# Kernel optimization log

Measured on AMD Instinct MI355X. Metric: run time of the kernel, lower is better.

## Reference

```python
import jax, jax.numpy as jnp
import numpy as np

B, S, IN_DIM, D, H, L, C = 8, 1024, 256, 1024, 16, 6, 10
DK = D // H
EPS = 1e-5


def setup_inputs() -> dict:
    key = jax.random.key(0)
    ks = iter(jax.random.split(key, 64))
    n = lambda shape, s=0.02: jax.random.normal(next(ks), shape, dtype=jnp.float32) * s
    inp = {
        'x': jax.random.normal(next(ks), (B, S, IN_DIM), dtype=jnp.float32),
        'emb_w': n((IN_DIM, D)), 'emb_b': jnp.zeros((D,), jnp.float32),
        'Wq': n((L, D, D)), 'bq': jnp.zeros((L, D), jnp.float32),
        'Wk': n((L, D, D)), 'bk': jnp.zeros((L, D), jnp.float32),
        'Wv': n((L, D, D)), 'bv': jnp.zeros((L, D), jnp.float32),
        'Wo': n((L, D, D)), 'bo': jnp.zeros((L, D), jnp.float32),
        'W1': n((L, D, 4 * D)), 'b1': jnp.zeros((L, 4 * D), jnp.float32),
        'W2': n((L, 4 * D, D)), 'b2': jnp.zeros((L, D), jnp.float32),
        'ln1_s': jnp.ones((L, D), jnp.float32), 'ln1_b': jnp.zeros((L, D), jnp.float32),
        'ln2_s': jnp.ones((L, D), jnp.float32), 'ln2_b': jnp.zeros((L, D), jnp.float32),
        'fc_w': n((D, C)), 'fc_b': jnp.zeros((C,), jnp.float32),
    }
    return inp


def _pos_encoding_rows(n_rows):
    # Faithful to the torch module: pe is [max_len,1,D]; pe[:x.size(0)] picks the
    # first `batch` positions and broadcasts over the sequence dim.
    pos = jnp.arange(n_rows, dtype=jnp.float32)[:, None]
    div = jnp.exp(jnp.arange(0, D, 2, dtype=jnp.float32) * (-np.log(10000.0) / D))
    pe = jnp.zeros((n_rows, D), jnp.float32)
    pe = pe.at[:, 0::2].set(jnp.sin(pos * div)).at[:, 1::2].set(jnp.cos(pos * div))
    return pe


def _layer_norm(x, scale, bias):
    mu = jnp.mean(x, axis=-1, keepdims=True)
    var = jnp.mean(jnp.square(x - mu), axis=-1, keepdims=True)
    return (x - mu) * jax.lax.rsqrt(var + EPS) * scale + bias


def reference(x, emb_w, emb_b, Wq, bq, Wk, bk, Wv, bv, Wo, bo,
              W1, b1, W2, b2, ln1_s, ln1_b, ln2_s, ln2_b, fc_w, fc_b):
    h = x @ emb_w + emb_b                              # [B,S,D]
    h = h + _pos_encoding_rows(B)[:, None, :]          # broadcast pe[:B] over seq
    scale = 1.0 / np.sqrt(DK)
    for i in range(L):
        def heads(y, W, b):
            return (y @ W + b).reshape(B, S, H, DK).transpose(0, 2, 1, 3)  # bhsd
        q = heads(h, Wq[i], bq[i])
        k = heads(h, Wk[i], bk[i])
        v = heads(h, Wv[i], bv[i])
        scores = jnp.einsum('bhqd,bhkd->bhqk', q, k) * scale
        p = jax.nn.softmax(scores, axis=-1)
        o = jnp.einsum('bhqk,bhkd->bhqd', p, v)
        o = o.transpose(0, 2, 1, 3).reshape(B, S, D)
        attn_out = o @ Wo[i] + bo[i]
        h = _layer_norm(h + attn_out, ln1_s[i], ln1_b[i])
        ff = jax.nn.relu(h @ W1[i] + b1[i]) @ W2[i] + b2[i]
        h = _layer_norm(h + ff, ln2_s[i], ln2_b[i])
    pooled = jnp.mean(h, axis=1)                       # [B,D]
    return pooled @ fc_w + fc_b                        # [B,C]
```

## Files before the change

kernel.cpp:

```cpp
#include <hip/hip_runtime.h>
#include <stdint.h>

#define B_   8
#define S_   1024
#define IND  256
#define D_   1024
#define H_   16
#define DKH  64
#define L_   6
#define FF   4096
#define NTOK (B_*S_)

typedef __bf16 bf16;
typedef __attribute__((ext_vector_type(4))) float  f32x4;
typedef __attribute__((ext_vector_type(8))) __bf16 bf16x8;
typedef __attribute__((ext_vector_type(4))) __bf16 bf16x4;
typedef __attribute__((ext_vector_type(2))) __bf16 bf16x2;

#define AS1 __attribute__((address_space(1)))
#define AS3 __attribute__((address_space(3)))

__device__ __forceinline__ void gload16(const void* g, void* l) {
  __builtin_amdgcn_global_load_lds((AS1 void*)(const_cast<void*>(g)), (AS3 void*)l, 16, 0, 0);
}

__global__ __launch_bounds__(256)
void k_trans(const float* __restrict__ in, bf16* __restrict__ out,
             int K, int N, long inStride, long outStride) {
  __shared__ float t[32][33];
  const float* inp = in + (long)blockIdx.z * inStride;
  bf16* outp = out + (long)blockIdx.z * outStride;
  const int n0 = blockIdx.x * 32, k0 = blockIdx.y * 32;
  const int tx = threadIdx.x & 31, ty = threadIdx.x >> 5;
  #pragma unroll
  for (int j = 0; j < 32; j += 8)
    t[ty + j][tx] = inp[(long)(k0 + ty + j) * N + n0 + tx];
  __syncthreads();
  #pragma unroll
  for (int j = 0; j < 32; j += 8)
    outp[(long)(n0 + ty + j) * K + k0 + tx] = (bf16)t[tx][ty + j];
}

__global__ __launch_bounds__(256)
void k_f2b(const float* __restrict__ in, bf16* __restrict__ out) {
  const long i = ((long)blockIdx.x * 256 + threadIdx.x) * 4;
  f32x4 v = *(const f32x4*)(in + i);
  bf16x4 o;
  #pragma unroll
  for (int j = 0; j < 4; ++j) o[j] = (bf16)v[j];
  *(bf16x4*)(out + i) = o;
}

__global__ __launch_bounds__(256)
void k_pe(float* __restrict__ pe) {
  const int i = blockIdx.x * 256 + threadIdx.x;
  const int b = i >> 10, d = i & 1023;
  const float k2 = (float)(d & ~1);
  const float dv = __expf(k2 * (-9.210340371976184f / (float)D_));
  const float a = (float)b * dv;
  pe[i] = (d & 1) ? cosf(a) : sinf(a);
}

__global__ __launch_bounds__(256)
void k_packb(const float* __restrict__ bq, const float* __restrict__ bk,
             const float* __restrict__ bv, float* __restrict__ out) {
  const int i = blockIdx.x * 256 + threadIdx.x;
  const int l = i / 3072, j = i % 3072;
  const float* src = (j < 1024) ? bq : ((j < 2048) ? bk : bv);
  out[i] = src[l * 1024 + (j & 1023)];
}

template<int EPI>
__global__ __launch_bounds__(256)
void k_gemm(const bf16* __restrict__ A, const bf16* __restrict__ Bt,
            const float* __restrict__ bias,
            void* __restrict__ out0, void* __restrict__ out1,
            const float* __restrict__ pe,
            int M, int N, int K) {
  __shared__ __align__(16) bf16 sA[128 * 32];
  __shared__ __align__(16) bf16 sB[128 * 32];
  const int tid = threadIdx.x;
  const int lane = tid & 63, wv = tid >> 6;
  const int bx = blockIdx.x, by = blockIdx.y;
  const int wm = wv >> 1, wn = wv & 1;
  const int lg = lane >> 4, lc = lane & 15;
  const long arow0 = (long)by * 128;
  const long brow0 = (long)bx * 128;
  const int c0 = (wv * 2 + 0) * 64 + lane;
  const int c1 = (wv * 2 + 1) * 64 + lane;
  const int r0 = c0 >> 2, s0 = c0 & 3;
  const int r1 = c1 >> 2, s1 = c1 & 3;
  bf16* ldsA0 = sA + (wv * 2 + 0) * 512;
  bf16* ldsA1 = sA + (wv * 2 + 1) * 512;
  bf16* ldsB0 = sB + (wv * 2 + 0) * 512;
  bf16* ldsB1 = sB + (wv * 2 + 1) * 512;
  const bf16* Ab = A + arow0 * K;
  const bf16* Bb = Bt + brow0 * K;
  f32x4 acc[4][4] = {};
  const int kT = K >> 5;
  for (int kt = 0; kt < kT; ++kt) {
    const int k0 = kt << 5;
    gload16(Ab + (long)r0 * K + k0 + s0 * 8, ldsA0);
    gload16(Ab + (long)r1 * K + k0 + s1 * 8, ldsA1);
    gload16(Bb + (long)r0 * K + k0 + s0 * 8, ldsB0);
    gload16(Bb + (long)r1 * K + k0 + s1 * 8, ldsB1);
    __syncthreads();
    bf16x8 af[4], bfr[4];
    #pragma unroll
    for (int mr = 0; mr < 4; ++mr)
      af[mr] = *(const bf16x8*)(sA + (wm * 64 + mr * 16 + lc) * 32 + lg * 8);
    #pragma unroll
    for (int nc = 0; nc < 4; ++nc)
      bfr[nc] = *(const bf16x8*)(sB + (wn * 64 + nc * 16 + lc) * 32 + lg * 8);
    #pragma unroll
    for (int mr = 0; mr < 4; ++mr)
      #pragma unroll
      for (int nc = 0; nc < 4; ++nc)
        acc[mr][nc] = __builtin_amdgcn_mfma_f32_16x16x32_bf16(af[mr], bfr[nc], acc[mr][nc], 0, 0, 0);
    __syncthreads();
  }
  #pragma unroll
  for (int mr = 0; mr < 4; ++mr) {
    const int row0 = by * 128 + wm * 64 + mr * 16 + lg * 4;
    #pragma unroll
    for (int nc = 0; nc < 4; ++nc) {
      const int col = bx * 128 + wn * 64 + nc * 16 + lc;
      const float bvv = bias[col];
      #pragma unroll
      for (int r = 0; r < 4; ++r) {
        float v = acc[mr][nc][r] + bvv;
        const long rr = row0 + r;
        if constexpr (EPI == 0) {
          ((bf16*)out0)[rr * N + col] = (bf16)v;
        } else {
          const long bb = rr >> 10;
          v += pe[bb * D_ + col];
          ((float*)out0)[rr * N + col] = v;
          ((bf16*)out1)[rr * N + col] = (bf16)v;
        }
      }
    }
  }
}

template<int EPI>
__global__ __launch_bounds__(512, 2)
void k_gemm256(const bf16* __restrict__ A, const bf16* __restrict__ Bt,
               const float* __restrict__ bias,
               void* __restrict__ out0, void* __restrict__ out1,
               int M, int N, int K) {
  __shared__ __align__(16) bf16 lds[65536];
  const int tid = threadIdx.x;
  const int lane = tid & 63, wv = tid >> 6;
  const int wm = wv >> 2, wn = wv & 3;
  const int lg = lane >> 4, lc = lane & 15;
  const int tileRow = blockIdx.y * 256, tileCol = blockIdx.x * 256;
  const bf16* Abase = A + (long)tileRow * K;
  const bf16* Bbase = Bt + (long)tileCol * K;
  const long laneOff = (long)lc * K + lg * 8;
  f32x4 acc[8][4] = {};
  const int NT = K >> 6;
  const int NI = NT >> 1;

  auto stA = [&](int t, int h, int bb) {
    const int rg = h * 16 + wv * 2;
    const int mb = rg >> 1;
    const bf16* s = Abase + (long)(mb * 16) * K + t * 64 + laneOff;
    bf16* d = lds + bb * 32768 + rg * 512;
    gload16(s, d);
    gload16(s + 32, d + 512);
  };
  auto stB = [&](int t, int h, int bb) {
    const int rg = h * 16 + wv * 2;
    const int mb = rg >> 1;
    const bf16* s = Bbase + (long)(mb * 16) * K + t * 64 + laneOff;
    bf16* d = lds + bb * 32768 + 16384 + rg * 512;
    gload16(s, d);
    gload16(s + 32, d + 512);
  };

  bf16x8 aF[8];
  bf16x8 bF0[4], bF1[4];

#define LDA(BB, MH) do { _Pragma("unroll") for (int m = 0; m < 4; ++m) \
    _Pragma("unroll") for (int kk = 0; kk < 2; ++kk) \
      aF[m*2+kk] = *(const bf16x8*)(lds + (BB)*32768 + ((wm*8 + (MH)*4 + m)*2 + kk)*512 + lane*8); \
  } while(0)
#define LDB(BB, NH, DST) do { _Pragma("unroll") for (int n = 0; n < 2; ++n) \
    _Pragma("unroll") for (int kk = 0; kk < 2; ++kk) \
      DST[n*2+kk] = *(const bf16x8*)(lds + (BB)*32768 + 16384 + ((wn*4 + (NH)*2 + n)*2 + kk)*512 + lane*8); \
  } while(0)
#define MM(MH, NH, BSRC, VM) do { \
    if ((VM) == 1) asm volatile("s_waitcnt vmcnt(4)" ::: "memory"); \
    if ((VM) == 2) asm volatile("s_waitcnt vmcnt(0)" ::: "memory"); \
    __builtin_amdgcn_s_barrier(); \
    __builtin_amdgcn_s_setprio(1); \
    _Pragma("unroll") for (int m = 0; m < 4; ++m) \
      _Pragma("unroll") for (int n = 0; n < 2; ++n) { \
        acc[(MH)*4+m][(NH)*2+n] = __builtin_amdgcn_mfma_f32_16x16x32_bf16(aF[m*2+0], BSRC[n*2+0], acc[(MH)*4+m][(NH)*2+n], 0, 0, 0); \
        acc[(MH)*4+m][(NH)*2+n] = __builtin_amdgcn_mfma_f32_16x16x32_bf16(aF[m*2+1], BSRC[n*2+1], acc[(MH)*4+m][(NH)*2+n], 0, 0, 0); \
      } \
    __builtin_amdgcn_s_setprio(0); \
    __builtin_amdgcn_s_barrier(); \
  } while(0)

  stA(0, 0, 0); stB(0, 0, 0); stA(0, 1, 0); stB(0, 1, 0);
  if (NT > 1) { stA(1, 0, 1); stB(1, 0, 1); }
  asm volatile("s_waitcnt vmcnt(4)" ::: "memory");
  __builtin_amdgcn_s_barrier();

  for (int i = 0; i < NI - 1; ++i) {
    const int t1 = 2 * i + 1, t2 = 2 * i + 2, t3 = 2 * i + 3;
    LDA(0, 0); LDB(0, 0, bF0); stA(t1, 1, 1); MM(0, 0, bF0, 0);
    LDB(0, 1, bF1);            stB(t1, 1, 1); MM(0, 1, bF1, 0);
    LDA(0, 1);                 stA(t2, 0, 0); MM(1, 0, bF0, 0);
                               stB(t2, 0, 0); MM(1, 1, bF1, 1);
    LDA(1, 0); LDB(1, 0, bF0); stA(t2, 1, 0); MM(0, 0, bF0, 0);
    LDB(1, 1, bF1);            stB(t2, 1, 0); MM(0, 1, bF1, 0);
    LDA(1, 1);                 stA(t3, 0, 1); MM(1, 0, bF0, 0);
                               stB(t3, 0, 1); MM(1, 1, bF1, 1);
  }
  {
    const int t1 = NT - 1;
    LDA(0, 0); LDB(0, 0, bF0); stA(t1, 1, 1); MM(0, 0, bF0, 0);
    LDB(0, 1, bF1);            stB(t1, 1, 1); MM(0, 1, bF1, 0);
    LDA(0, 1);                                MM(1, 0, bF0, 0);
                                              MM(1, 1, bF1, 2);
    LDA(1, 0); LDB(1, 0, bF0);                MM(0, 0, bF0, 0);
    LDB(1, 1, bF1);                           MM(0, 1, bF1, 0);
    LDA(1, 1);                                MM(1, 0, bF0, 0);
                                              MM(1, 1, bF1, 0);
  }
#undef LDA
#undef LDB
#undef MM

  #pragma unroll
  for (int mr = 0; mr < 8; ++mr) {
    const int row0 = tileRow + wm * 128 + mr * 16 + lg * 4;
    #pragma unroll
    for (int nr = 0; nr < 4; ++nr) {
      const int col = tileCol + wn * 64 + nr * 16 + lc;
      const float bvv = bias[col];
      if constexpr (EPI == 2) {
        const int which = col >> 10;
        const int hh = (col & 1023) >> 6;
        const int dk = col & 63;
        const long bb = row0 >> 10;
        const int sr = row0 & 1023;
        if (which == 2) {
          bf16x4 pk;
          #pragma unroll
          for (int r = 0; r < 4; ++r) pk[r] = (bf16)(acc[mr][nr][r] + bvv);
          *(bf16x4*)((bf16*)out1 + ((bb * H_ + hh) * (long)DKH + dk) * S_ + sr) = pk;
        } else {
          #pragma unroll
          for (int r = 0; r < 4; ++r) {
            float v = acc[mr][nr][r] + bvv;
            if (which == 0) v *= 0.125f;
            ((bf16*)out0)[(long)which * NTOK * D_ + ((bb * H_ + hh) * (long)S_ + sr + r) * DKH + dk] = (bf16)v;
          }
        }
      } else {
        #pragma unroll
        for (int r = 0; r < 4; ++r) {
          float v = acc[mr][nr][r] + bvv;
          const long rr = row0 + r;
          if constexpr (EPI == 1) v = fmaxf(v, 0.f);
          ((bf16*)out0)[rr * N + col] = (bf16)v;
        }
      }
    }
  }
}

__global__ __launch_bounds__(256)
void k_flash(const bf16* __restrict__ qg, const bf16* __restrict__ kgl,
             const bf16* __restrict__ vtg, bf16* __restrict__ og) {
  __shared__ __align__(16) bf16 sK[64 * 64];
  __shared__ __align__(16) bf16 sV[64 * 64];
  __shared__ __align__(16) bf16 sP[4 * 16 * 64];
  const int tid = threadIdx.x, lane = tid & 63, wv = tid >> 6;
  const int lg = lane >> 4, lc = lane & 15;
  const int bh = blockIdx.y, qt = blockIdx.x;
  const long base = (long)bh * S_ * DKH;
  const bf16* qb = qg + base;
  const bf16* kb = kgl + base;
  const bf16* vb = vtg + base;
  const int qrow = qt * 64 + wv * 16 + lc;
  const bf16x8 qf0 = *(const bf16x8*)(qb + (long)qrow * DKH + lg * 8);
  const bf16x8 qf1 = *(const bf16x8*)(qb + (long)qrow * DKH + 32 + lg * 8);
  float mrun = -3e38f, lrun = 0.f;
  f32x4 oacc[4] = {};
  bf16* sPw = sP + wv * (16 * 64);
  const int swzP = (lc & 7) << 4;
  const int c0 = wv * 128 + lane, c1 = c0 + 64;
  const int r0 = c0 >> 3, sl0 = (c0 & 7) ^ (r0 & 7);
  const int r1 = c1 >> 3, sl1 = (c1 & 7) ^ (r1 & 7);
  bf16* dst0 = sK + c0 * 8 - lane * 8;
  bf16* dst1 = sK + c1 * 8 - lane * 8;
  bf16* dstV0 = sV + c0 * 8 - lane * 8;
  bf16* dstV1 = sV + c1 * 8 - lane * 8;
  for (int kt = 0; kt < S_ / 64; ++kt) {
    const int gk = kt * 64;
    gload16(kb + (long)(gk + r0) * DKH + sl0 * 8, dst0);
    gload16(kb + (long)(gk + r1) * DKH + sl1 * 8, dst1);
    gload16(vb + (long)r0 * S_ + gk + sl0 * 8, dstV0);
    gload16(vb + (long)r1 * S_ + gk + sl1 * 8, dstV1);
    __syncthreads();
    f32x4 sacc[4] = {};
    #pragma unroll
    for (int nc = 0; nc < 4; ++nc) {
      const int kr = nc * 16 + lc;
      bf16x8 k0 = *(const bf16x8*)((char*)sK + kr * 128 + (((0 + lg) ^ (kr & 7)) << 4));
      bf16x8 k1 = *(const bf16x8*)((char*)sK + kr * 128 + (((4 + lg) ^ (kr & 7)) << 4));
      sacc[nc] = __builtin_amdgcn_mfma_f32_16x16x32_bf16(k0, qf0, sacc[nc], 0, 0, 0);
      sacc[nc] = __builtin_amdgcn_mfma_f32_16x16x32_bf16(k1, qf1, sacc[nc], 0, 0, 0);
    }
    float pm = sacc[0][0];
    #pragma unroll
    for (int nc = 0; nc < 4; ++nc)
      #pragma unroll
      for (int r = 0; r < 4; ++r) pm = fmaxf(pm, sacc[nc][r]);
    pm = fmaxf(pm, __shfl_xor(pm, 16));
    pm = fmaxf(pm, __shfl_xor(pm, 32));
    const float mnew = fmaxf(mrun, pm);
    const float fac = __expf(mrun - mnew);
    float ps = 0.f;
    #pragma unroll
    for (int nc = 0; nc < 4; ++nc)
      #pragma unroll
      for (int r = 0; r < 4; ++r) {
        const float p = __expf(sacc[nc][r] - mnew);
        sacc[nc][r] = p;
        ps += p;
      }
    ps += __shfl_xor(ps, 16);
    ps += __shfl_xor(ps, 32);
    lrun = lrun * fac + ps;
    mrun = mnew;
    #pragma unroll
    for (int nc = 0; nc < 4; ++nc)
      #pragma unroll
      for (int rp = 0; rp < 2; ++rp) {
        bf16x2 t;
        t[0] = (bf16)sacc[nc][rp * 2 + 0];
        t[1] = (bf16)sacc[nc][rp * 2 + 1];
        *(bf16x2*)((char*)sPw + lc * 128 + ((nc * 32 + lg * 8 + rp * 4) ^ swzP)) = t;
      }
    asm volatile("s_waitcnt lgkmcnt(0)" ::: "memory");
    __builtin_amdgcn_sched_barrier(0);
    float fr[4];
    #pragma unroll
    for (int r = 0; r < 4; ++r) fr[r] = __shfl(fac, lg * 4 + r);
    #pragma unroll
    for (int nc = 0; nc < 4; ++nc)
      #pragma unroll
      for (int r = 0; r < 4; ++r) oacc[nc][r] *= fr[r];
    #pragma unroll
    for (int m = 0; m < 2; ++m) {
      const bf16x8 pf = *(const bf16x8*)((char*)sPw + lc * 128 + ((m * 64 + lg * 16) ^ swzP));
      #pragma unroll
      for (int nc = 0; nc < 4; ++nc) {
        const int vr = nc * 16 + lc;
        bf16x8 vf = *(const bf16x8*)((char*)sV + vr * 128 + (((m * 4 + lg) ^ (vr & 7)) << 4));
        oacc[nc] = __builtin_amdgcn_mfma_f32_16x16x32_bf16(pf, vf, oacc[nc], 0, 0, 0);
      }
    }
    __syncthreads();
  }
  const int b = bh >> 4, h = bh & 15;
  const float linv = 1.f / lrun;
  #pragma unroll
  for (int r = 0; r < 4; ++r) {
    const float inv = __shfl(linv, lg * 4 + r);
    const int s = qt * 64 + wv * 16 + lg * 4 + r;
    const long obase = (((long)b * S_ + s) * H_ + h) * DKH;
    #pragma unroll
    for (int nc = 0; nc < 4; ++nc)
      og[obase + nc * 16 + lc] = (bf16)(oacc[nc][r] * inv);
  }
}

__global__ __launch_bounds__(256)
void k_addln(const float* __restrict__ hin, const bf16* __restrict__ dlt,
             const float* __restrict__ sc, const float* __restrict__ bi,
             float* __restrict__ hout, bf16* __restrict__ hbout) {
  const int row = blockIdx.x, t = threadIdx.x;
  const long off = (long)row * D_ + t * 4;
  f32x4 hv = *(const f32x4*)(hin + off);
  bf16x4 dv = *(const bf16x4*)(dlt + off);
  f32x4 x;
  float s = 0.f, ss = 0.f;
  #pragma unroll
  for (int j = 0; j < 4; ++j) { x[j] = hv[j] + (float)dv[j]; s += x[j]; ss += x[j] * x[j]; }
  #pragma unroll
  for (int m = 1; m < 64; m <<= 1) { s += __shfl_xor(s, m); ss += __shfl_xor(ss, m); }
  __shared__ float red[8];
  const int w = t >> 6, ln = t & 63;
  if (ln == 0) { red[w] = s; red[4 + w] = ss; }
  __syncthreads();
  s = red[0] + red[1] + red[2] + red[3];
  ss = red[4] + red[5] + red[6] + red[7];
  const float mu = s * (1.f / D_);
  const float rstd = rsqrtf(ss * (1.f / D_) - mu * mu + 1e-5f);
  f32x4 scv = *(const f32x4*)(sc + t * 4);
  f32x4 biv = *(const f32x4*)(bi + t * 4);
  f32x4 y; bf16x4 yb;
  #pragma unroll
  for (int j = 0; j < 4; ++j) { y[j] = (x[j] - mu) * rstd * scv[j] + biv[j]; yb[j] = (bf16)y[j]; }
  *(f32x4*)(hout + off) = y;
  *(bf16x4*)(hbout + off) = yb;
}

__global__ __launch_bounds__(256)
void k_pool1(const float* __restrict__ h, float* __restrict__ part) {
  const int i = blockIdx.x * 256 + threadIdx.x;
  const int b = i >> 10, d = i & 1023;
  const int s0 = blockIdx.y * 128;
  float s = 0.f;
  for (int t = 0; t < 128; ++t) s += h[((long)b * S_ + s0 + t) * D_ + d];
  part[(long)blockIdx.y * NTOK + i] = s;
}

__global__ __launch_bounds__(256)
void k_pool2(const float* __restrict__ part, float* __restrict__ pooled) {
  const int i = blockIdx.x * 256 + threadIdx.x;
  float s = 0.f;
  #pragma unroll
  for (int j = 0; j < 8; ++j) s += part[(long)j * NTOK + i];
  pooled[i] = s * (1.f / S_);
}

__global__ __launch_bounds__(64)
void k_fc(const float* __restrict__ pooled, const float* __restrict__ fw,
          const float* __restrict__ fb, float* __restrict__ out) {
  const int b = blockIdx.x / 10, c = blockIdx.x % 10;
  const int lane = threadIdx.x;
  float s = 0.f;
  for (int d = lane; d < D_; d += 64) s += pooled[b * D_ + d] * fw[d * 10 + c];
  #pragma unroll
  for (int m = 1; m < 64; m <<= 1) s += __shfl_xor(s, m);
  if (lane == 0) out[b * 10 + c] = s + fb[c];
}

extern "C" void kernel_launch(void* const* d_in, const int* in_sizes, int n_in,
                              void* d_out, int out_size, void* d_ws, size_t ws_size,
                              hipStream_t stream) {
  const float* x     = (const float*)d_in[0];
  const float* emb_w = (const float*)d_in[1];
  const float* emb_b = (const float*)d_in[2];
  const float* Wq    = (const float*)d_in[3];
  const float* bq    = (const float*)d_in[4];
  const float* Wk    = (const float*)d_in[5];
  const float* bk    = (const float*)d_in[6];
  const float* Wv    = (const float*)d_in[7];
  const float* bv    = (const float*)d_in[8];
  const float* Wo    = (const float*)d_in[9];
  const float* bo    = (const float*)d_in[10];
  const float* W1    = (const float*)d_in[11];
  const float* b1    = (const float*)d_in[12];
  const float* W2    = (const float*)d_in[13];
  const float* b2    = (const float*)d_in[14];
  const float* ln1s  = (const float*)d_in[15];
  const float* ln1b  = (const float*)d_in[16];
  const float* ln2s  = (const float*)d_in[17];
  const float* ln2b  = (const float*)d_in[18];
  const float* fcw   = (const float*)d_in[19];
  const float* fcb   = (const float*)d_in[20];

  char* w = (char*)d_ws;
  size_t off = 0;
  auto alloc = [&](size_t bytes) -> char* {
    char* p = w + off;
    off += (bytes + 255) & ~(size_t)255;
    return p;
  };
  bf16*  x_bf  = (bf16*) alloc((size_t)NTOK * IND * 2);
  bf16*  embT  = (bf16*) alloc((size_t)D_ * IND * 2);
  bf16*  qkvT  = (bf16*) alloc((size_t)L_ * 3 * D_ * D_ * 2);
  bf16*  woT   = (bf16*) alloc((size_t)L_ * D_ * D_ * 2);
  bf16*  w1T   = (bf16*) alloc((size_t)L_ * FF * D_ * 2);
  bf16*  w2T   = (bf16*) alloc((size_t)L_ * D_ * FF * 2);
  float* qkvB  = (float*)alloc((size_t)L_ * 3 * D_ * 4);
  float* pe    = (float*)alloc((size_t)B_ * D_ * 4);
  float* h_f   = (float*)alloc((size_t)NTOK * D_ * 4);
  bf16*  h_b   = (bf16*) alloc((size_t)NTOK * D_ * 2);
  bf16*  delta = (bf16*) alloc((size_t)NTOK * D_ * 2);
  float* pooled= (float*)alloc((size_t)B_ * D_ * 4);
  float* part  = (float*)alloc((size_t)8 * NTOK * 4);
  bf16*  scratch = (bf16*)alloc((size_t)NTOK * FF * 2);
  bf16* qb  = scratch;
  bf16* kb  = scratch + (size_t)NTOK * D_;
  bf16* vTb = scratch + (size_t)2 * NTOK * D_;
  bf16* ob  = scratch + (size_t)3 * NTOK * D_;
  bf16* ffn1 = scratch;
  (void)ws_size; (void)in_sizes; (void)n_in; (void)out_size;

  k_f2b<<<dim3(NTOK * IND / 1024), dim3(256), 0, stream>>>(x, x_bf);
  k_trans<<<dim3(D_ / 32, IND / 32, 1), dim3(256), 0, stream>>>(emb_w, embT, IND, D_, 0, 0);
  k_trans<<<dim3(32, 32, L_), dim3(256), 0, stream>>>(Wq, qkvT,               D_, D_, (long)D_ * D_, (long)3 * D_ * D_);
  k_trans<<<dim3(32, 32, L_), dim3(256), 0, stream>>>(Wk, qkvT + D_ * D_,     D_, D_, (long)D_ * D_, (long)3 * D_ * D_);
  k_trans<<<dim3(32, 32, L_), dim3(256), 0, stream>>>(Wv, qkvT + 2 * D_ * D_, D_, D_, (long)D_ * D_, (long)3 * D_ * D_);
  k_trans<<<dim3(32, 32, L_), dim3(256), 0, stream>>>(Wo, woT, D_, D_, (long)D_ * D_, (long)D_ * D_);
  k_trans<<<dim3(FF / 32, 32, L_), dim3(256), 0, stream>>>(W1, w1T, D_, FF, (long)D_ * FF, (long)FF * D_);
  k_trans<<<dim3(32, FF / 32, L_), dim3(256), 0, stream>>>(W2, w2T, FF, D_, (long)FF * D_, (long)D_ * FF);
  k_pe<<<dim3(B_ * D_ / 256), dim3(256), 0, stream>>>(pe);
  k_packb<<<dim3(L_ * 3 * D_ / 256), dim3(256), 0, stream>>>(bq, bk, bv, qkvB);

  k_gemm<3><<<dim3(D_ / 128, NTOK / 128), dim3(256), 0, stream>>>(
      x_bf, embT, emb_b, h_f, h_b, pe, NTOK, D_, IND);

  for (int l = 0; l < L_; ++l) {
    k_gemm256<2><<<dim3(3 * D_ / 256, NTOK / 256), dim3(512), 0, stream>>>(
        h_b, qkvT + (size_t)l * 3 * D_ * D_, qkvB + l * 3 * D_,
        qb, vTb, NTOK, 3 * D_, D_);
    k_flash<<<dim3(S_ / 64, B_ * H_), dim3(256), 0, stream>>>(qb, kb, vTb, ob);
    k_gemm256<0><<<dim3(D_ / 256, NTOK / 256), dim3(512), 0, stream>>>(
        ob, woT + (size_t)l * D_ * D_, bo + l * D_,
        delta, nullptr, NTOK, D_, D_);
    k_addln<<<dim3(NTOK), dim3(256), 0, stream>>>(h_f, delta, ln1s + l * D_, ln1b + l * D_, h_f, h_b);
    k_gemm256<1><<<dim3(FF / 256, NTOK / 256), dim3(512), 0, stream>>>(
        h_b, w1T + (size_t)l * FF * D_, b1 + l * FF,
        ffn1, nullptr, NTOK, FF, D_);
    k_gemm256<0><<<dim3(D_ / 256, NTOK / 256), dim3(512), 0, stream>>>(
        ffn1, w2T + (size_t)l * D_ * FF, b2 + l * D_,
        delta, nullptr, NTOK, D_, FF);
    k_addln<<<dim3(NTOK), dim3(256), 0, stream>>>(h_f, delta, ln2s + l * D_, ln2b + l * D_, h_f, h_b);
  }

  k_pool1<<<dim3(NTOK / 256, 8), dim3(256), 0, stream>>>(h_f, part);
  k_pool2<<<dim3(NTOK / 256), dim3(256), 0, stream>>>(part, pooled);
  k_fc<<<dim3(B_ * 10), dim3(64), 0, stream>>>(pooled, fcw, fcb, (float*)d_out);
}
```

Baseline: 2.656 ms.

## Remap workgroups for XCD locality, retile N=1024 GEMMs, deepen 256-tile prefetch

Adds an XCD-aware block-index remap to both GEMM kernels and the flash-attention kernel, so consecutive tiles land on the same chiplet and share L2. The N=1024 GEMMs (Wo and W2) move from 256x256 tiles (128 blocks) to 128x128 tiles (512 blocks) to fill more CUs. The 256-tile GEMM pipeline is reordered to prefetch a full K-tile ahead, using vmcnt(8) waits and fewer barriers. The 128-tile GEMM also gets a new LDS layout matching the 256 kernel's fragment layout. The trade-offs are that smaller tiles lower data reuse per block, and the W2 GEMM with K=4096 runs on a simple kernel with no double buffering.

```diff
diff --git a/kernel.cpp b/kernel.cpp
--- a/kernel.cpp
+++ b/kernel.cpp
@@ -72,59 +72,57 @@
 
 template<int EPI>
 __global__ __launch_bounds__(256)
-void k_gemm(const bf16* __restrict__ A, const bf16* __restrict__ Bt,
-            const float* __restrict__ bias,
-            void* __restrict__ out0, void* __restrict__ out1,
-            const float* __restrict__ pe,
-            int M, int N, int K) {
+void k_gemm128(const bf16* __restrict__ A, const bf16* __restrict__ Bt,
+               const float* __restrict__ bias,
+               void* __restrict__ out0, void* __restrict__ out1,
+               const float* __restrict__ pe,
+               int M, int N, int K) {
   __shared__ __align__(16) bf16 sA[128 * 32];
   __shared__ __align__(16) bf16 sB[128 * 32];
-  const int tid = threadIdx.x;
-  const int lane = tid & 63, wv = tid >> 6;
-  const int bx = blockIdx.x, by = blockIdx.y;
+  const int tid = threadIdx.x, lane = tid & 63, wv = tid >> 6;
   const int wm = wv >> 1, wn = wv & 1;
   const int lg = lane >> 4, lc = lane & 15;
-  const long arow0 = (long)by * 128;
-  const long brow0 = (long)bx * 128;
-  const int c0 = (wv * 2 + 0) * 64 + lane;
-  const int c1 = (wv * 2 + 1) * 64 + lane;
-  const int r0 = c0 >> 2, s0 = c0 & 3;
-  const int r1 = c1 >> 2, s1 = c1 & 3;
-  bf16* ldsA0 = sA + (wv * 2 + 0) * 512;
-  bf16* ldsA1 = sA + (wv * 2 + 1) * 512;
-  bf16* ldsB0 = sB + (wv * 2 + 0) * 512;
-  bf16* ldsB1 = sB + (wv * 2 + 1) * 512;
-  const bf16* Ab = A + arow0 * K;
-  const bf16* Bb = Bt + brow0 * K;
+  const int gx = gridDim.x;
+  const int nwg = gx * gridDim.y;
+  int bid = blockIdx.x + blockIdx.y * gx;
+  const int cpx = nwg >> 3;
+  bid = (bid & 7) * cpx + (bid >> 3);
+  const int bxs = bid % gx, bys = bid / gx;
+  const int tileRow = bys * 128, tileCol = bxs * 128;
+  const bf16* Abase = A + (long)tileRow * K;
+  const bf16* Bbase = Bt + (long)tileCol * K;
+  const long laneOff = (long)lc * K + lg * 8;
   f32x4 acc[4][4] = {};
-  const int kT = K >> 5;
-  for (int kt = 0; kt < kT; ++kt) {
-    const int k0 = kt << 5;
-    gload16(Ab + (long)r0 * K + k0 + s0 * 8, ldsA0);
-    gload16(Ab + (long)r1 * K + k0 + s1 * 8, ldsA1);
-    gload16(Bb + (long)r0 * K + k0 + s0 * 8, ldsB0);
-    gload16(Bb + (long)r1 * K + k0 + s1 * 8, ldsB1);
+  const int NT = K >> 5;
+  const int rg = wv * 2;
+  for (int t = 0; t < NT; ++t) {
+    const bf16* sa = Abase + (long)(rg * 16) * K + t * 32 + laneOff;
+    const bf16* sb = Bbase + (long)(rg * 16) * K + t * 32 + laneOff;
+    gload16(sa,                sA + rg * 512);
+    gload16(sa + (long)16 * K, sA + rg * 512 + 512);
+    gload16(sb,                sB + rg * 512);
+    gload16(sb + (long)16 * K, sB + rg * 512 + 512);
     __syncthreads();
-    bf16x8 af[4], bfr[4];
+    bf16x8 aF[4], bF[4];
     #pragma unroll
     for (int mr = 0; mr < 4; ++mr)
-      af[mr] = *(const bf16x8*)(sA + (wm * 64 + mr * 16 + lc) * 32 + lg * 8);
+      aF[mr] = *(const bf16x8*)(sA + (wm * 4 + mr) * 512 + lane * 8);
     #pragma unroll
     for (int nc = 0; nc < 4; ++nc)
-      bfr[nc] = *(const bf16x8*)(sB + (wn * 64 + nc * 16 + lc) * 32 + lg * 8);
+      bF[nc] = *(const bf16x8*)(sB + (wn * 4 + nc) * 512 + lane * 8);
     #pragma unroll
     for (int mr = 0; mr < 4; ++mr)
       #pragma unroll
       for (int nc = 0; nc < 4; ++nc)
-        acc[mr][nc] = __builtin_amdgcn_mfma_f32_16x16x32_bf16(af[mr], bfr[nc], acc[mr][nc], 0, 0, 0);
+        acc[mr][nc] = __builtin_amdgcn_mfma_f32_16x16x32_bf16(aF[mr], bF[nc], acc[mr][nc], 0, 0, 0);
     __syncthreads();
   }
   #pragma unroll
   for (int mr = 0; mr < 4; ++mr) {
-    const int row0 = by * 128 + wm * 64 + mr * 16 + lg * 4;
+    const int row0 = tileRow + wm * 64 + mr * 16 + lg * 4;
     #pragma unroll
     for (int nc = 0; nc < 4; ++nc) {
-      const int col = bx * 128 + wn * 64 + nc * 16 + lc;
+      const int col = tileCol + wn * 64 + nc * 16 + lc;
       const float bvv = bias[col];
       #pragma unroll
       for (int r = 0; r < 4; ++r) {
@@ -154,7 +152,13 @@
   const int lane = tid & 63, wv = tid >> 6;
   const int wm = wv >> 2, wn = wv & 3;
   const int lg = lane >> 4, lc = lane & 15;
-  const int tileRow = blockIdx.y * 256, tileCol = blockIdx.x * 256;
+  const int gx = gridDim.x;
+  const int nwg = gx * gridDim.y;
+  int bid = blockIdx.x + blockIdx.y * gx;
+  const int cpx = nwg >> 3;
+  bid = (bid & 7) * cpx + (bid >> 3);
+  const int bxs = bid % gx, bys = bid / gx;
+  const int tileRow = bys * 256, tileCol = bxs * 256;
   const bf16* Abase = A + (long)tileRow * K;
   const bf16* Bbase = Bt + (long)tileCol * K;
   const long laneOff = (long)lc * K + lg * 8;
@@ -190,10 +194,7 @@
     _Pragma("unroll") for (int kk = 0; kk < 2; ++kk) \
       DST[n*2+kk] = *(const bf16x8*)(lds + (BB)*32768 + 16384 + ((wn*4 + (NH)*2 + n)*2 + kk)*512 + lane*8); \
   } while(0)
-#define MM(MH, NH, BSRC, VM) do { \
-    if ((VM) == 1) asm volatile("s_waitcnt vmcnt(4)" ::: "memory"); \
-    if ((VM) == 2) asm volatile("s_waitcnt vmcnt(0)" ::: "memory"); \
-    __builtin_amdgcn_s_barrier(); \
+#define MMA(MH, NH, BSRC) do { \
     __builtin_amdgcn_s_setprio(1); \
     _Pragma("unroll") for (int m = 0; m < 4; ++m) \
       _Pragma("unroll") for (int n = 0; n < 2; ++n) { \
@@ -201,39 +202,41 @@
         acc[(MH)*4+m][(NH)*2+n] = __builtin_amdgcn_mfma_f32_16x16x32_bf16(aF[m*2+1], BSRC[n*2+1], acc[(MH)*4+m][(NH)*2+n], 0, 0, 0); \
       } \
     __builtin_amdgcn_s_setprio(0); \
-    __builtin_amdgcn_s_barrier(); \
   } while(0)
+#define VM8 asm volatile("s_waitcnt vmcnt(8)" ::: "memory")
+#define VM0 asm volatile("s_waitcnt vmcnt(0)" ::: "memory")
+#define BAR __builtin_amdgcn_s_barrier()
 
   stA(0, 0, 0); stB(0, 0, 0); stA(0, 1, 0); stB(0, 1, 0);
-  if (NT > 1) { stA(1, 0, 1); stB(1, 0, 1); }
-  asm volatile("s_waitcnt vmcnt(4)" ::: "memory");
-  __builtin_amdgcn_s_barrier();
+  stA(1, 0, 1); stB(1, 0, 1); stA(1, 1, 1); stB(1, 1, 1);
 
   for (int i = 0; i < NI - 1; ++i) {
-    const int t1 = 2 * i + 1, t2 = 2 * i + 2, t3 = 2 * i + 3;
-    LDA(0, 0); LDB(0, 0, bF0); stA(t1, 1, 1); MM(0, 0, bF0, 0);
-    LDB(0, 1, bF1);            stB(t1, 1, 1); MM(0, 1, bF1, 0);
-    LDA(0, 1);                 stA(t2, 0, 0); MM(1, 0, bF0, 0);
-                               stB(t2, 0, 0); MM(1, 1, bF1, 1);
-    LDA(1, 0); LDB(1, 0, bF0); stA(t2, 1, 0); MM(0, 0, bF0, 0);
-    LDB(1, 1, bF1);            stB(t2, 1, 0); MM(0, 1, bF1, 0);
-    LDA(1, 1);                 stA(t3, 0, 1); MM(1, 0, bF0, 0);
-                               stB(t3, 0, 1); MM(1, 1, bF1, 1);
+    const int t2 = 2 * i + 2, t3 = 2 * i + 3;
+    VM8; BAR; LDA(0, 0); LDB(0, 0, bF0);                    MMA(0, 0, bF0);
+         BAR; LDB(0, 1, bF1); stA(t2, 0, 0);                MMA(0, 1, bF1);
+         BAR; LDA(0, 1);      stB(t2, 0, 0);                MMA(1, 0, bF0);
+         BAR;                 stA(t2, 1, 0); stB(t2, 1, 0); MMA(1, 1, bF1);
+    VM8; BAR; LDA(1, 0); LDB(1, 0, bF0);                    MMA(0, 0, bF0);
+         BAR; LDB(1, 1, bF1); stA(t3, 0, 1);                MMA(0, 1, bF1);
+         BAR; LDA(1, 1);      stB(t3, 0, 1);                MMA(1, 0, bF0);
+         BAR;                 stA(t3, 1, 1); stB(t3, 1, 1); MMA(1, 1, bF1);
   }
   {
-    const int t1 = NT - 1;
-    LDA(0, 0); LDB(0, 0, bF0); stA(t1, 1, 1); MM(0, 0, bF0, 0);
-    LDB(0, 1, bF1);            stB(t1, 1, 1); MM(0, 1, bF1, 0);
-    LDA(0, 1);                                MM(1, 0, bF0, 0);
-                                              MM(1, 1, bF1, 2);
-    LDA(1, 0); LDB(1, 0, bF0);                MM(0, 0, bF0, 0);
-    LDB(1, 1, bF1);                           MM(0, 1, bF1, 0);
-    LDA(1, 1);                                MM(1, 0, bF0, 0);
-                                              MM(1, 1, bF1, 0);
+    VM8; BAR; LDA(0, 0); LDB(0, 0, bF0); MMA(0, 0, bF0);
+         BAR; LDB(0, 1, bF1);            MMA(0, 1, bF1);
+         BAR; LDA(0, 1);                 MMA(1, 0, bF0);
+         BAR;                            MMA(1, 1, bF1);
+    VM0; BAR; LDA(1, 0); LDB(1, 0, bF0); MMA(0, 0, bF0);
+         BAR; LDB(1, 1, bF1);            MMA(0, 1, bF1);
+         BAR; LDA(1, 1);                 MMA(1, 0, bF0);
+         BAR;                            MMA(1, 1, bF1);
   }
 #undef LDA
 #undef LDB
-#undef MM
+#undef MMA
+#undef VM8
+#undef VM0
+#undef BAR
 
   #pragma unroll
   for (int mr = 0; mr < 8; ++mr) {
@@ -282,7 +285,9 @@
   __shared__ __align__(16) bf16 sP[4 * 16 * 64];
   const int tid = threadIdx.x, lane = tid & 63, wv = tid >> 6;
   const int lg = lane >> 4, lc = lane & 15;
-  const int bh = blockIdx.y, qt = blockIdx.x;
+  int bid = blockIdx.x + blockIdx.y * 16;
+  bid = (bid & 7) * 256 + (bid >> 3);
+  const int qt = bid & 15, bh = bid >> 4;
   const long base = (long)bh * S_ * DKH;
   const bf16* qb = qg + base;
   const bf16* kb = kgl + base;
@@ -508,7 +513,7 @@
   k_pe<<<dim3(B_ * D_ / 256), dim3(256), 0, stream>>>(pe);
   k_packb<<<dim3(L_ * 3 * D_ / 256), dim3(256), 0, stream>>>(bq, bk, bv, qkvB);
 
-  k_gemm<3><<<dim3(D_ / 128, NTOK / 128), dim3(256), 0, stream>>>(
+  k_gemm128<3><<<dim3(D_ / 128, NTOK / 128), dim3(256), 0, stream>>>(
       x_bf, embT, emb_b, h_f, h_b, pe, NTOK, D_, IND);
 
   for (int l = 0; l < L_; ++l) {
@@ -516,16 +521,16 @@
         h_b, qkvT + (size_t)l * 3 * D_ * D_, qkvB + l * 3 * D_,
         qb, vTb, NTOK, 3 * D_, D_);
     k_flash<<<dim3(S_ / 64, B_ * H_), dim3(256), 0, stream>>>(qb, kb, vTb, ob);
-    k_gemm256<0><<<dim3(D_ / 256, NTOK / 256), dim3(512), 0, stream>>>(
+    k_gemm128<0><<<dim3(D_ / 128, NTOK / 128), dim3(256), 0, stream>>>(
         ob, woT + (size_t)l * D_ * D_, bo + l * D_,
-        delta, nullptr, NTOK, D_, D_);
+        delta, nullptr, nullptr, NTOK, D_, D_);
     k_addln<<<dim3(NTOK), dim3(256), 0, stream>>>(h_f, delta, ln1s + l * D_, ln1b + l * D_, h_f, h_b);
     k_gemm256<1><<<dim3(FF / 256, NTOK / 256), dim3(512), 0, stream>>>(
         h_b, w1T + (size_t)l * FF * D_, b1 + l * FF,
         ffn1, nullptr, NTOK, FF, D_);
-    k_gemm256<0><<<dim3(D_ / 256, NTOK / 256), dim3(512), 0, stream>>>(
+    k_gemm128<0><<<dim3(D_ / 128, NTOK / 128), dim3(256), 0, stream>>>(
         ffn1, w2T + (size_t)l * D_ * FF, b2 + l * D_,
-        delta, nullptr, NTOK, D_, FF);
+        delta, nullptr, nullptr, NTOK, D_, FF);
     k_addln<<<dim3(NTOK), dim3(256), 0, stream>>>(h_f, delta, ln2s + l * D_, ln2b + l * D_, h_f, h_b);
   }
 
```

Result: slower. 2.726 ms (+2.6%).
